# Kernel tuning notes

Measured on AMD Instinct MI355X. Metric: run time of the kernel, lower is better.

The kernel has to match this reference:

```python
import math
import jax, jax.numpy as jnp
import numpy as np

MIN_AMT, MAX_AMT = 1, 32
C = 3
B, H, W = 128, 224, 224


def build_kernel_table():
    # kernels[i] has size = i + MIN_AMT: vertical center column, each channel sums to 1,
    # zero-padded (centered) to MAX_AMT x MAX_AMT (pad_to_width).
    tbl = np.zeros((MAX_AMT - MIN_AMT + 1, MAX_AMT, MAX_AMT, C), np.float32)
    for i, size in enumerate(range(MIN_AMT, MAX_AMT + 1)):
        pad = MAX_AMT - size
        t = pad // 2
        col = t + size // 2
        tbl[i, t:t + size, col, :] = 1.0 / size
    return jnp.asarray(tbl)


def setup_inputs() -> dict:
    key = jax.random.key(0)
    k1, k2, k3 = jax.random.split(key, 3)
    x = jax.random.uniform(k1, (B, H, W, C), jnp.float32)  # image batch
    amt = jax.random.randint(k2, (B,), MIN_AMT, MAX_AMT, dtype=jnp.int32)  # [min, max)
    angles = jax.random.randint(k3, (B,), 0, 91, dtype=jnp.int32)  # degrees [0, 91)
    return {"x": x, "kernels_table": build_kernel_table(), "amt": amt, "angles": angles}


def _rotate_nearest(img, rad):
    # img: (K, K, C); nearest-neighbor rotation about image center (tf.contrib.image.rotate
    # convention: output (x,y) samples input at [cos -sin; sin cos] @ (x,y) + centering offset).
    K = img.shape[0]
    cos, sin = jnp.cos(rad), jnp.sin(rad)
    coords = jnp.arange(K, dtype=jnp.float32)
    yy, xx = jnp.meshgrid(coords, coords, indexing="ij")
    e = jnp.float32(K - 1)
    x_off = (e - (cos * e - sin * e)) * 0.5
    y_off = (e - (sin * e + cos * e)) * 0.5
    sx = cos * xx - sin * yy + x_off
    sy = sin * xx + cos * yy + y_off
    ix = jnp.round(sx).astype(jnp.int32)
    iy = jnp.round(sy).astype(jnp.int32)
    valid = (ix >= 0) & (ix < K) & (iy >= 0) & (iy < K)
    g = img[jnp.clip(iy, 0, K - 1), jnp.clip(ix, 0, K - 1)]  # (K, K, C)
    return jnp.where(valid[..., None], g, jnp.float32(0.0))


def _depthwise_conv(img, ker):
    # img: (H, W, C); ker: (K, K, C) -> per-channel SAME conv, stride 1.
    out = jax.lax.conv_general_dilated(
        img[None], ker[:, :, None, :], (1, 1), "SAME",
        dimension_numbers=("NHWC", "HWIO", "NHWC"), feature_group_count=C)
    return out[0]


def reference(x, kernels_table, amt, angles):
    ker = kernels_table[amt]                                # (B, K, K, C) per-sample gather
    rad = angles.astype(jnp.float32) * jnp.float32(math.pi / 180.0)
    ker = jax.vmap(_rotate_nearest)(ker, rad)               # per-sample rotation
    out = jax.vmap(_depthwise_conv)(x, ker)                 # per-sample depthwise conv
    return out.reshape(-1, 224, 224, 3)
```

## Files before the change

kernel.cpp:

```cpp
#include <hip/hip_runtime.h>
#include <math.h>

namespace {

constexpr int Himg = 224, Wimg = 224, Cn = 3, Kk = 32;
constexpr int MAXT = 64;
constexpr int WSTRIDE = 512;
constexpr int IMG_F  = Himg * Wimg * Cn;
constexpr int ROW_F  = Wimg * Cn;
constexpr int ROW_B  = ROW_F * 4;

constexpr int IN_CH  = 144;
constexpr int ED_CH  = 24;
constexpr int IN_PER_IMG = Himg * IN_CH;
constexpr int ED_PER_IMG = Himg * ED_CH;
constexpr int IN_BLK = IN_PER_IMG / 256;
constexpr int ED_BLK = ED_PER_IMG / 256;
constexpr int BLK_PER_IMG = IN_BLK + ED_BLK;
constexpr int FAST_LO = 9, FAST_HI = 117;

typedef float v4  __attribute__((ext_vector_type(4), aligned(4)));
typedef float v4a __attribute__((ext_vector_type(4), aligned(16)));


__global__ __launch_bounds__(64)
void build_taps(const float* __restrict__ tbl,
                const int* __restrict__ amt,
                const int* __restrict__ ang,
                int* __restrict__ ws)
{
    const int b   = blockIdx.x;
    const int tid = threadIdx.x;

    __shared__ int   s_cnt;
    __shared__ float s_w;
    __shared__ int   s_dky[MAXT], s_dkx[MAXT];

    if (tid == 0) { s_cnt = 0; s_w = 0.0f; }
    __syncthreads();

    const int a = amt[b];
    const float  rad = (float)ang[b] * (float)(M_PI / 180.0);
    const double rd  = (double)rad;
    const float  cth = (float)cos(rd);
    const float  sth = (float)sin(rd);
    const float  e   = 31.0f;
    const float xoff = __fmul_rn(__fsub_rn(e, __fsub_rn(__fmul_rn(cth, e), __fmul_rn(sth, e))), 0.5f);
    const float yoff = __fmul_rn(__fsub_rn(e, __fadd_rn(__fmul_rn(sth, e), __fmul_rn(cth, e))), 0.5f);

    for (int p = tid; p < Kk * Kk; p += 64) {
        const int   ky = p >> 5, kx = p & 31;
        const float xf = (float)kx, yf = (float)ky;
        const float sx = __fadd_rn(__fsub_rn(__fmul_rn(cth, xf), __fmul_rn(sth, yf)), xoff);
        const float sy = __fadd_rn(__fadd_rn(__fmul_rn(sth, xf), __fmul_rn(cth, yf)), yoff);
        const int ix = (int)rintf(sx);
        const int iy = (int)rintf(sy);
        if (ix >= 0 && ix < Kk && iy >= 0 && iy < Kk) {
            const float v = tbl[((a * Kk + iy) * Kk + ix) * Cn];
            if (v != 0.0f) {
                const int idx = atomicAdd(&s_cnt, 1);
                if (idx < MAXT) {
                    s_dky[idx] = ky - 15;
                    s_dkx[idx] = kx - 15;
                    s_w = v;
                }
            }
        }
    }
    __syncthreads();

    const int n = min(s_cnt, MAXT);
    int* wsb = ws + b * WSTRIDE;
    if (tid == 0) { wsb[0] = n; wsb[1] = __float_as_int(s_w); }
    for (int i = tid; i < n; i += 64) {
        wsb[2 + i]   = s_dky[i];
        wsb[66 + i]  = s_dkx[i];
        wsb[130 + i] = s_dky[i] * ROW_B + s_dkx[i] * (int)(Cn * sizeof(float));
    }
}

__global__ __launch_bounds__(256)
void blur_direct(const float* __restrict__ x,
                 const int* __restrict__ ws,
                 float* __restrict__ out,
                 int B)
{
    const int tid = threadIdx.x;
    const int L   = blockIdx.x;

    int b, c;
    if (B == 128) {
        const int xcd = L & 7;
        const int j   = L >> 3;
        const int g   = j / BLK_PER_IMG;
        c = j - g * BLK_PER_IMG;
        b = g * 8 + xcd;
    } else {
        b = L / BLK_PER_IMG;
        c = L - b * BLK_PER_IMG;
    }

    __shared__ int shNW[2];
    __shared__ int s_dky[MAXT], s_dkx[MAXT], s_xoff[MAXT];
    const int* wsb = ws + b * WSTRIDE;
    if (tid < 2)    shNW[tid]   = wsb[tid];
    if (tid < MAXT) {
        s_dky[tid]  = wsb[2 + tid];
        s_dkx[tid]  = wsb[66 + tid];
        s_xoff[tid] = wsb[130 + tid];
    }
    __syncthreads();

    const int   n = shNW[0];
    const float w = __int_as_float(shNW[1]);
    const float* xb = x + (size_t)b * IMG_F;

    if (c < IN_BLK) {
        const int ii = c * 256 + tid;
        const int y  = ii / IN_CH;
        const int k  = ii - y * IN_CH + 12;
        const int fbase = y * ROW_F + 4 * k;
        const char* base = (const char*)xb + (size_t)fbase * 4;

        float a0 = 0.0f, a1 = 0.0f, a2 = 0.0f, a3 = 0.0f;

        if (c >= FAST_LO && c < FAST_HI) {
            int i = 0;
            for (; i + 4 <= n; i += 4) {
                const v4 f0 = *(const v4*)(base + s_xoff[i]);
                const v4 f1 = *(const v4*)(base + s_xoff[i + 1]);
                const v4 f2 = *(const v4*)(base + s_xoff[i + 2]);
                const v4 f3 = *(const v4*)(base + s_xoff[i + 3]);
                a0 += f0.x; a1 += f0.y; a2 += f0.z; a3 += f0.w;
                a0 += f1.x; a1 += f1.y; a2 += f1.z; a3 += f1.w;
                a0 += f2.x; a1 += f2.y; a2 += f2.z; a3 += f2.w;
                a0 += f3.x; a1 += f3.y; a2 += f3.z; a3 += f3.w;
            }
            for (; i < n; ++i) {
                const v4 f = *(const v4*)(base + s_xoff[i]);
                a0 += f.x; a1 += f.y; a2 += f.z; a3 += f.w;
            }
        } else {
            for (int i = 0; i < n; ++i) {
                const int  row = y + s_dky[i];
                const bool ok  = (unsigned)row < (unsigned)Himg;
                const int  off = ok ? s_xoff[i] : 0;
                const float m  = ok ? 1.0f : 0.0f;
                const v4 f = *(const v4*)(base + off);
                a0 += m * f.x; a1 += m * f.y; a2 += m * f.z; a3 += m * f.w;
            }
        }

        float* o = out + (size_t)b * IMG_F + fbase;
        __builtin_nontemporal_store(v4a{a0 * w, a1 * w, a2 * w, a3 * w}, (v4a*)o);
    } else {
        const int ee = (c - IN_BLK) * 256 + tid;
        const int y  = ee / ED_CH;
        const int j  = ee - y * ED_CH;
        const int k  = (j < 12) ? j : (j + 144);
        const int fd0 = 4 * k;

        float acc[4] = {0.0f, 0.0f, 0.0f, 0.0f};
        for (int i = 0; i < n; ++i) {
            const int  row = y + s_dky[i];
            const bool rok = (unsigned)row < (unsigned)Himg;
            const int  s0  = fd0 + 3 * s_dkx[i];
            const int  ob  = row * ROW_F + s0;
#pragma unroll
            for (int q = 0; q < 4; ++q) {
                const bool ok  = rok & ((unsigned)(s0 + q) < (unsigned)ROW_F);
                const int  off = ok ? (ob + q) : 0;
                const float v  = xb[off];
                acc[q] += ok ? v : 0.0f;
            }
        }

        float* o = out + (size_t)b * IMG_F + (size_t)y * ROW_F + fd0;
        __builtin_nontemporal_store(
            v4a{acc[0] * w, acc[1] * w, acc[2] * w, acc[3] * w}, (v4a*)o);
    }
}

}

extern "C" void kernel_launch(void* const* d_in, const int* in_sizes, int n_in,
                              void* d_out, int out_size, void* d_ws, size_t ws_size,
                              hipStream_t stream) {
    const float* x   = (const float*)d_in[0];
    const float* tbl = (const float*)d_in[1];
    const int*   amt = (const int*)d_in[2];
    const int*   ang = (const int*)d_in[3];
    float*       out = (float*)d_out;
    int*         ws  = (int*)d_ws;

    const int B = in_sizes[2];

    build_taps<<<B, 64, 0, stream>>>(tbl, amt, ang, ws);
    blur_direct<<<B * BLK_PER_IMG, 256, 0, stream>>>(x, ws, out, B);
}
```

Before: 227.5 us.

## Pre-pad image into RGBX layout with margins before tap-sum blur

Adds a pass that copies each image into a padded 4-float-per-pixel buffer with 16-pixel horizontal zero margins, then runs a per-pixel blur that uses aligned 16-byte loads and needs no horizontal bounds checks. The goal is to simplify the inner loop and remove the separate edge-handling blocks. In exchange it adds a full extra write and read of a larger intermediate buffer. The original direct kernel is kept as a fallback when the workspace is too small.

```diff
diff --git a/kernel.cpp b/kernel.cpp
--- a/kernel.cpp
+++ b/kernel.cpp
@@ -10,14 +10,21 @@
 constexpr int ROW_F  = Wimg * Cn;
 constexpr int ROW_B  = ROW_F * 4;
 
+constexpr int PR_PX  = 256;
+constexpr int PR_B   = PR_PX * 16;
+constexpr int PIMG_B = Himg * PR_B;
+constexpr size_t TAPS_BYTES = 128 * WSTRIDE * sizeof(int);
+
+constexpr int PADBLK  = Himg * PR_PX / 256;
+constexpr int CONVBLK = Himg * Wimg / 256;
+constexpr int FAST_LO = 14, FAST_HI = 182;
+
 constexpr int IN_CH  = 144;
 constexpr int ED_CH  = 24;
-constexpr int IN_PER_IMG = Himg * IN_CH;
-constexpr int ED_PER_IMG = Himg * ED_CH;
-constexpr int IN_BLK = IN_PER_IMG / 256;
-constexpr int ED_BLK = ED_PER_IMG / 256;
+constexpr int IN_BLK = Himg * IN_CH / 256;
+constexpr int ED_BLK = Himg * ED_CH / 256;
 constexpr int BLK_PER_IMG = IN_BLK + ED_BLK;
-constexpr int FAST_LO = 9, FAST_HI = 117;
+constexpr int FB_FAST_LO = 9, FB_FAST_HI = 117;
 
 typedef float v4  __attribute__((ext_vector_type(4), aligned(4)));
 typedef float v4a __attribute__((ext_vector_type(4), aligned(16)));
@@ -75,8 +82,100 @@
     for (int i = tid; i < n; i += 64) {
         wsb[2 + i]   = s_dky[i];
         wsb[66 + i]  = s_dkx[i];
-        wsb[130 + i] = s_dky[i] * ROW_B + s_dkx[i] * (int)(Cn * sizeof(float));
-    }
+        wsb[130 + i] = (s_dky[i] << 12) + (s_dkx[i] << 4);
+        wsb[194 + i] = s_dky[i] * ROW_B + s_dkx[i] * (int)(Cn * 4);
+    }
+}
+
+__global__ __launch_bounds__(256)
+void pad_rgbx(const float* __restrict__ x, float* __restrict__ pad, int B)
+{
+    const int L = blockIdx.x, tid = threadIdx.x;
+    int b, c;
+    if (B == 128) {
+        const int xcd = L & 7;
+        const int j   = L >> 3;
+        const int g   = j / PADBLK;
+        c = j - g * PADBLK; b = g * 8 + xcd;
+    } else { b = L / PADBLK; c = L - b * PADBLK; }
+
+    const int p  = c * 256 + tid;
+    const int y  = p >> 8;
+    const int px = p & 255;
+    const int sx = px - 16;
+    const bool ok = (unsigned)sx < (unsigned)Wimg;
+
+    const float* s = x + (size_t)b * IMG_F + ((size_t)y * Wimg + (ok ? sx : 0)) * Cn;
+    const float m  = ok ? 1.0f : 0.0f;
+    const float v0 = s[0], v1 = s[1], v2 = s[2];
+
+    v4a* d = (v4a*)((char*)pad + (size_t)b * PIMG_B + (size_t)y * PR_B + ((size_t)px << 4));
+    *d = v4a{v0 * m, v1 * m, v2 * m, 0.0f};
+}
+
+__global__ __launch_bounds__(256)
+void blur_rgbx(const float* __restrict__ pad,
+               const int* __restrict__ ws,
+               float* __restrict__ out,
+               int B)
+{
+    const int L = blockIdx.x, tid = threadIdx.x;
+    int b, c;
+    if (B == 128) {
+        const int xcd = L & 7;
+        const int j   = L >> 3;
+        const int g   = j / CONVBLK;
+        c = j - g * CONVBLK; b = g * 8 + xcd;
+    } else { b = L / CONVBLK; c = L - b * CONVBLK; }
+
+    __shared__ int shNW[2];
+    __shared__ int s_dky[MAXT], s_poff[MAXT];
+    const int* wsb = ws + b * WSTRIDE;
+    if (tid < 2)    shNW[tid] = wsb[tid];
+    if (tid < MAXT) { s_dky[tid] = wsb[2 + tid]; s_poff[tid] = wsb[130 + tid]; }
+    __syncthreads();
+
+    const int   n = shNW[0];
+    const float w = __int_as_float(shNW[1]);
+
+    const int p  = c * 256 + tid;
+    const int y  = p / 224;
+    const int px = p - y * 224;
+
+    const char* base = (const char*)pad + (size_t)b * PIMG_B
+                     + (size_t)y * PR_B + ((size_t)(px + 16) << 4);
+
+    float a0 = 0.0f, a1 = 0.0f, a2 = 0.0f;
+
+    if (c >= FAST_LO && c < FAST_HI) {
+        int i = 0;
+        for (; i + 4 <= n; i += 4) {
+            const v4 f0 = *(const v4*)(base + s_poff[i]);
+            const v4 f1 = *(const v4*)(base + s_poff[i + 1]);
+            const v4 f2 = *(const v4*)(base + s_poff[i + 2]);
+            const v4 f3 = *(const v4*)(base + s_poff[i + 3]);
+            a0 += f0.x; a1 += f0.y; a2 += f0.z;
+            a0 += f1.x; a1 += f1.y; a2 += f1.z;
+            a0 += f2.x; a1 += f2.y; a2 += f2.z;
+            a0 += f3.x; a1 += f3.y; a2 += f3.z;
+        }
+        for (; i < n; ++i) {
+            const v4 f = *(const v4*)(base + s_poff[i]);
+            a0 += f.x; a1 += f.y; a2 += f.z;
+        }
+    } else {
+        for (int i = 0; i < n; ++i) {
+            const int  row = y + s_dky[i];
+            const bool ok  = (unsigned)row < (unsigned)Himg;
+            const int  off = ok ? s_poff[i] : 0;
+            const float m  = ok ? 1.0f : 0.0f;
+            const v4 f = *(const v4*)(base + off);
+            a0 += m * f.x; a1 += m * f.y; a2 += m * f.z;
+        }
+    }
+
+    float* o = out + (size_t)b * IMG_F + (size_t)p * 3;
+    o[0] = a0 * w; o[1] = a1 * w; o[2] = a2 * w;
 }
 
 __global__ __launch_bounds__(256)
@@ -95,19 +194,16 @@
         const int g   = j / BLK_PER_IMG;
         c = j - g * BLK_PER_IMG;
         b = g * 8 + xcd;
-    } else {
-        b = L / BLK_PER_IMG;
-        c = L - b * BLK_PER_IMG;
-    }
+    } else { b = L / BLK_PER_IMG; c = L - b * BLK_PER_IMG; }
 
     __shared__ int shNW[2];
     __shared__ int s_dky[MAXT], s_dkx[MAXT], s_xoff[MAXT];
     const int* wsb = ws + b * WSTRIDE;
-    if (tid < 2)    shNW[tid]   = wsb[tid];
+    if (tid < 2)    shNW[tid] = wsb[tid];
     if (tid < MAXT) {
         s_dky[tid]  = wsb[2 + tid];
         s_dkx[tid]  = wsb[66 + tid];
-        s_xoff[tid] = wsb[130 + tid];
+        s_xoff[tid] = wsb[194 + tid];
     }
     __syncthreads();
 
@@ -124,7 +220,7 @@
 
         float a0 = 0.0f, a1 = 0.0f, a2 = 0.0f, a3 = 0.0f;
 
-        if (c >= FAST_LO && c < FAST_HI) {
+        if (c >= FB_FAST_LO && c < FB_FAST_HI) {
             int i = 0;
             for (; i + 4 <= n; i += 4) {
                 const v4 f0 = *(const v4*)(base + s_xoff[i]);
@@ -196,5 +292,13 @@
     const int B = in_sizes[2];
 
     build_taps<<<B, 64, 0, stream>>>(tbl, amt, ang, ws);
-    blur_direct<<<B * BLK_PER_IMG, 256, 0, stream>>>(x, ws, out, B);
-}
+
+    const size_t need = TAPS_BYTES + (size_t)B * PIMG_B;
+    if (ws_size >= need) {
+        float* pad = (float*)((char*)d_ws + TAPS_BYTES);
+        pad_rgbx<<<B * PADBLK, 256, 0, stream>>>(x, pad, B);
+        blur_rgbx<<<B * CONVBLK, 256, 0, stream>>>(pad, ws, out, B);
+    } else {
+        blur_direct<<<B * BLK_PER_IMG, 256, 0, stream>>>(x, ws, out, B);
+    }
+}
```

New measurement: 234.3 us. 1.03x slower.
